# Kernel tuning notes

Hardware: AMD Instinct MI355X
Metric: run time of the kernel (lower is better)

The kernel has to match this reference:

```python
import jax, jax.numpy as jnp
import numpy as np

B, L, D = 2, 2048, 768
HEADS, KEY, HEAD = 12, 64, 64


def _glorot(key, shape):
    fan_in, fan_out = shape[0], shape[1]
    lim = jnp.sqrt(6.0 / (fan_in + fan_out))
    return jax.random.uniform(key, shape, jnp.float32, -lim, lim)


def setup_inputs() -> dict:
    key = jax.random.key(0)
    ks = jax.random.split(key, 8)
    return {
        "q": jax.random.normal(ks[0], (B, L, D), jnp.float32),
        "k": jax.random.normal(ks[1], (B, L, D), jnp.float32),
        "v": jax.random.normal(ks[2], (B, L, D), jnp.float32),
        "att_mask": jnp.ones((B, L), jnp.float32),
        "Wq": _glorot(ks[3], (D, HEADS * KEY)),
        "bq": jnp.zeros((HEADS * KEY,), jnp.float32),
        "Wk": _glorot(ks[4], (D, HEADS * KEY)),
        "bk": jnp.zeros((HEADS * KEY,), jnp.float32),
        "Wv": _glorot(ks[5], (D, HEADS * HEAD)),
        "bv": jnp.zeros((HEADS * HEAD,), jnp.float32),
        "Wo": _glorot(ks[6], (HEADS * HEAD, HEADS * HEAD)),
        "bo": jnp.zeros((HEADS * HEAD,), jnp.float32),
    }


def reference(q, k, v, att_mask, Wq, bq, Wk, bk, Wv, bv, Wo, bo):
    b, lq, _ = q.shape
    lk = k.shape[1]
    # att_mask [B,Lk] -> [B,Lq,Lk] via ones outer product (as in the TF code)
    mask2d = jnp.ones((b, lq, 1), jnp.float32) * att_mask[:, None, :]
    qh = (q @ Wq + bq).reshape(b, lq, HEADS, KEY)
    kh = (k @ Wk + bk).reshape(b, lk, HEADS, KEY)
    vh = (v @ Wv + bv).reshape(b, lk, HEADS, HEAD)
    # scores [B,H,Lq,Lk]
    a = jnp.einsum('binh,bjnh->bnij', qh, kh) / (KEY ** 0.5)
    a = a + (1.0 - mask2d[:, None, :, :]) * -99999.0
    a = jax.nn.softmax(a, axis=-1)
    o = jnp.einsum('bnij,bjnh->binh', a, vh).reshape(b, lq, HEADS * HEAD)
    return o @ Wo + bo
```

## Files before the change

kernel.cpp:

```cpp
#include <hip/hip_runtime.h>
#include <math.h>

#define BB 2
#define LL 2048
#define DD 768
#define NH 12
#define HD 64
#define EL (4096*768)
#define WEL (768*768)

typedef __attribute__((ext_vector_type(8))) short short8;
typedef __attribute__((ext_vector_type(4))) float f32x4;
typedef __attribute__((ext_vector_type(16))) float f32x16;
typedef __attribute__((ext_vector_type(4))) unsigned int u32x4;
typedef unsigned short ushortT;

union U8 { unsigned short u[8]; short8 v; };
union UB { u32x4 u; short8 v; };

#define MFMA(a,b,c)   __builtin_amdgcn_mfma_f32_16x16x32_bf16((a),(b),(c),0,0,0)
#define MFMA32(a,b,c) __builtin_amdgcn_mfma_f32_32x32x16_bf16((a),(b),(c),0,0,0)

__device__ inline unsigned short f2bf(float x) {
    unsigned int u = __float_as_uint(x);
    unsigned int r = (u + 0x7fffu + ((u >> 16) & 1u)) >> 16;
    return (unsigned short)r;
}
__device__ inline float bf2f(unsigned short s) {
    return __uint_as_float(((unsigned int)s) << 16);
}
__device__ inline void split2(float x, unsigned short& h, unsigned short& l) {
    h = f2bf(x);
    l = f2bf(x - bf2f(h));
}
__device__ inline int swz(int row) { return (((row & 7) ^ ((row >> 3) & 7)) << 4); }

__device__ inline void gl2lds16(const void* g, void* l) {
    __builtin_amdgcn_global_load_lds((__attribute__((address_space(1))) const void*)g,
                                     (__attribute__((address_space(3))) void*)l, 16, 0, 0);
}

struct SplitArgs { const float* src[3]; ushortT* dh[3]; ushortT* dl[3]; };
__global__ __launch_bounds__(256) void split_plain(SplitArgs a)
{
    const int z = blockIdx.y;
    const size_t i = ((size_t)blockIdx.x * 256 + threadIdx.x) * 8;
    const float* s = a.src[z];
    float4 v0 = *reinterpret_cast<const float4*>(s + i);
    float4 v1 = *reinterpret_cast<const float4*>(s + i + 4);
    float f[8] = {v0.x, v0.y, v0.z, v0.w, v1.x, v1.y, v1.z, v1.w};
    U8 h, l;
    #pragma unroll
    for (int j = 0; j < 8; ++j) split2(f[j], h.u[j], l.u[j]);
    *reinterpret_cast<short8*>(a.dh[z] + i) = h.v;
    *reinterpret_cast<short8*>(a.dl[z] + i) = l.v;
}

struct WArgs { const float* src[4]; ushortT* dh[4]; ushortT* dl[4]; float scale[4]; };
__global__ __launch_bounds__(256) void split_wt(WArgs a)
{
    const int n  = blockIdx.x * 256 + threadIdx.x;
    const int k0 = blockIdx.y * 8;
    const int z  = blockIdx.z;
    const float* W = a.src[z];
    const float sc = a.scale[z];
    U8 h, l;
    #pragma unroll
    for (int j = 0; j < 8; ++j) {
        float x = W[(size_t)(k0 + j) * DD + n] * sc;
        split2(x, h.u[j], l.u[j]);
    }
    *reinterpret_cast<short8*>(a.dh[z] + (size_t)n * DD + k0) = h.v;
    *reinterpret_cast<short8*>(a.dl[z] + (size_t)n * DD + k0) = l.v;
}

template<int MODE>
__global__ __launch_bounds__(256) void gemm_mfma(const ushortT* __restrict__ Ah, size_t apb,
                                                 const ushortT* __restrict__ Bth, size_t bpb,
                                                 const float* __restrict__ bias, float bscale,
                                                 float* __restrict__ outF,
                                                 ushortT* __restrict__ outH,
                                                 ushortT* __restrict__ outL)
{
    __shared__ ushortT As[64 * 64];
    __shared__ ushortT Bs[64 * 64];

    const int tid  = threadIdx.x;
    const int lane = tid & 63;
    const int w    = tid >> 6;
    const int g    = lane >> 4, c = lane & 15;
    const int n0   = blockIdx.x * 64;
    const int m0   = blockIdx.y * 64;

    const int srow0 = w * 16 + (lane >> 3);
    const int csrc  = (lane & 7) ^ (lane >> 3);
    const size_t plA = (csrc >= 4) ? apb : 0;
    const size_t plB = (csrc >= 4) ? bpb : 0;
    const size_t abase = (size_t)(m0 + srow0) * (DD * 2) + plA + (size_t)(csrc & 3) * 16;
    const size_t bbase = (size_t)(n0 + srow0) * (DD * 2) + plB + (size_t)(csrc & 3) * 16;

    f32x4 acc[4] = {{0,0,0,0},{0,0,0,0},{0,0,0,0},{0,0,0,0}};

    const int arow = w * 16 + c;
    const int ahc  = g ^ (arow & 7);
    const int aoff_h = arow * 64 + ahc * 8;
    const int aoff_l = arow * 64 + (ahc ^ 4) * 8;

    for (int kt = 0; kt < DD / 32; ++kt) {
        const size_t ko = (size_t)kt * 64;
        const char* asrc = (const char*)Ah  + abase + ko;
        const char* bsrc = (const char*)Bth + bbase + ko;
        gl2lds16(asrc,                &As[w * 1024]);
        gl2lds16(asrc + 8 * (DD * 2), &As[w * 1024 + 512]);
        gl2lds16(bsrc,                &Bs[w * 1024]);
        gl2lds16(bsrc + 8 * (DD * 2), &Bs[w * 1024 + 512]);
        __syncthreads();

        const short8 a_h = *reinterpret_cast<const short8*>(&As[aoff_h]);
        const short8 a_l = *reinterpret_cast<const short8*>(&As[aoff_l]);
        #pragma unroll
        for (int nf = 0; nf < 4; ++nf) {
            const int brow = nf * 16 + c;
            const int bhc  = g ^ (brow & 7);
            const short8 b_h = *reinterpret_cast<const short8*>(&Bs[brow * 64 + bhc * 8]);
            const short8 b_l = *reinterpret_cast<const short8*>(&Bs[brow * 64 + (bhc ^ 4) * 8]);
            acc[nf] = MFMA(a_h, b_h, acc[nf]);
            acc[nf] = MFMA(a_l, b_h, acc[nf]);
            acc[nf] = MFMA(a_h, b_l, acc[nf]);
        }
        __syncthreads();
    }

    #pragma unroll
    for (int nf = 0; nf < 4; ++nf) {
        const int n = n0 + nf * 16 + c;
        const float bz = bias[n] * bscale;
        #pragma unroll
        for (int r = 0; r < 4; ++r) {
            const int m = m0 + w * 16 + 4 * g + r;
            const float vv = acc[nf][r] + bz;
            if (MODE == 0) {
                outF[(size_t)m * DD + n] = vv;
            } else {
                unsigned short hh, ll;
                split2(vv, hh, ll);
                outH[(size_t)m * DD + n] = hh;
                outL[(size_t)m * DD + n] = ll;
            }
        }
    }
}

__global__ __launch_bounds__(128) void attn_mfma(const ushortT* __restrict__ Qh_g,
                                                 const ushortT* __restrict__ Ql_g,
                                                 const ushortT* __restrict__ Kh_g,
                                                 const ushortT* __restrict__ Kl_g,
                                                 const ushortT* __restrict__ Vh_g,
                                                 const ushortT* __restrict__ Vl_g,
                                                 const float* __restrict__ mask,
                                                 ushortT* __restrict__ Oh_g,
                                                 ushortT* __restrict__ Ol_g)
{
    __shared__ ushortT Kh[32 * 64];
    __shared__ ushortT Kl[32 * 64];
    __shared__ ushortT Vt[64 * 64];
    __shared__ float mterm[32];

    const int tid  = threadIdx.x;
    const int lane = tid & 63;
    const int w    = tid >> 6;
    const int qc   = lane & 31;
    const int h5   = lane >> 5;
    const int bh   = blockIdx.y;
    const int b    = bh / NH;
    const int h    = bh % NH;
    const int r0   = blockIdx.x * 64;
    const int qrow = r0 + w * 32 + qc;

    short8 qbh[4], qbl[4];
    {
        const size_t qoff = (size_t)(b * LL + qrow) * DD + h * 64;
        #pragma unroll
        for (int ks = 0; ks < 4; ++ks) {
            const int d0 = 8 * h5 + 16 * ks;
            qbh[ks] = *reinterpret_cast<const short8*>(Qh_g + qoff + d0);
            qbl[ks] = *reinterpret_cast<const short8*>(Ql_g + qoff + d0);
        }
    }

    f32x16 Oa[2];
    #pragma unroll
    for (int m = 0; m < 2; ++m)
        #pragma unroll
        for (int r = 0; r < 16; ++r) Oa[m][r] = 0.f;
    float mrun = -1e30f, lrun = 0.f;

    const int skey = tid >> 2;
    const int sd0v = (tid & 3) * 16;
    ushortT* kdst = w ? Kl : Kh;
    const ushortT* ksrcp = w ? Kl_g : Kh_g;
    const int krow_l = lane >> 3;
    const int kcsrc  = (lane & 7) ^ krow_l;

    for (int kt = 0; kt < LL / 32; ++kt) {
        __syncthreads();
        {
            const size_t kbase = (size_t)(b * LL + kt * 32 + krow_l) * DD + h * 64 + kcsrc * 8;
            #pragma unroll
            for (int t = 0; t < 4; ++t)
                gl2lds16(ksrcp + kbase + (size_t)(8 * t) * DD, kdst + t * 512);
        }
        {
            const size_t vo = (size_t)(b * LL + kt * 32 + skey) * DD + h * 64 + sd0v;
            U8 a0, a1, b0, b1;
            a0.v = *reinterpret_cast<const short8*>(Vh_g + vo);
            a1.v = *reinterpret_cast<const short8*>(Vh_g + vo + 8);
            b0.v = *reinterpret_cast<const short8*>(Vl_g + vo);
            b1.v = *reinterpret_cast<const short8*>(Vl_g + vo + 8);
            #pragma unroll
            for (int j = 0; j < 8; ++j) {
                int d = sd0v + j; int s = swz(d);
                Vt[d * 64 + (((2 * skey) ^ s) >> 1)]      = a0.u[j];
                Vt[d * 64 + (((64 + 2 * skey) ^ s) >> 1)] = b0.u[j];
                d = sd0v + 8 + j; s = swz(d);
                Vt[d * 64 + (((2 * skey) ^ s) >> 1)]      = a1.u[j];
                Vt[d * 64 + (((64 + 2 * skey) ^ s) >> 1)] = b1.u[j];
            }
        }
        if (tid < 32)
            mterm[tid] = (1.0f - mask[(size_t)b * LL + kt * 32 + tid]) * -99999.0f;
        __syncthreads();

        f32x16 sa;
        #pragma unroll
        for (int r = 0; r < 16; ++r) sa[r] = 0.f;
        #pragma unroll
        for (int ks = 0; ks < 4; ++ks) {
            const int ch = (h5 + 2 * ks) ^ (qc & 7);
            const short8 kfh = *reinterpret_cast<const short8*>(&Kh[qc * 64 + ch * 8]);
            const short8 kfl = *reinterpret_cast<const short8*>(&Kl[qc * 64 + ch * 8]);
            sa = MFMA32(kfh, qbh[ks], sa);
            sa = MFMA32(kfl, qbh[ks], sa);
            sa = MFMA32(kfh, qbl[ks], sa);
        }

        float sm[16];
        #pragma unroll
        for (int r = 0; r < 16; ++r)
            sm[r] = sa[r] + mterm[(r & 3) + 8 * (r >> 2) + 4 * h5];
        float tm = sm[0];
        #pragma unroll
        for (int r = 1; r < 16; ++r) tm = fmaxf(tm, sm[r]);
        tm = fmaxf(tm, __shfl_xor(tm, 32));
        const float mn = fmaxf(mrun, tm);
        const float scale = __expf(mrun - mn);
        float p[16];
        float rs = 0.f;
        #pragma unroll
        for (int r = 0; r < 16; ++r) { p[r] = __expf(sm[r] - mn); rs += p[r]; }
        rs += __shfl_xor(rs, 32);
        lrun = lrun * scale + rs;
        mrun = mn;
        #pragma unroll
        for (int m = 0; m < 2; ++m)
            #pragma unroll
            for (int r = 0; r < 16; ++r) Oa[m][r] *= scale;

        unsigned int pkh[8], pkl[8], xph[8], xpl[8];
        #pragma unroll
        for (int s2 = 0; s2 < 8; ++s2) {
            unsigned short h0, l0, h1, l1;
            split2(p[2 * s2],     h0, l0);
            split2(p[2 * s2 + 1], h1, l1);
            pkh[s2] = (unsigned int)h0 | ((unsigned int)h1 << 16);
            pkl[s2] = (unsigned int)l0 | ((unsigned int)l1 << 16);
            xph[s2] = __shfl_xor(pkh[s2], 32);
            xpl[s2] = __shfl_xor(pkl[s2], 32);
        }
        UB pbh[2], pbl[2];
        if (h5 == 0) {
            pbh[0].u = (u32x4){pkh[0], pkh[1], xph[0], xph[1]};
            pbl[0].u = (u32x4){pkl[0], pkl[1], xpl[0], xpl[1]};
            pbh[1].u = (u32x4){pkh[4], pkh[5], xph[4], xph[5]};
            pbl[1].u = (u32x4){pkl[4], pkl[5], xpl[4], xpl[5]};
        } else {
            pbh[0].u = (u32x4){xph[2], xph[3], pkh[2], pkh[3]};
            pbl[0].u = (u32x4){xpl[2], xpl[3], pkl[2], pkl[3]};
            pbh[1].u = (u32x4){xph[6], xph[7], pkh[6], pkh[7]};
            pbl[1].u = (u32x4){xpl[6], xpl[7], pkl[6], pkl[7]};
        }

        #pragma unroll
        for (int m = 0; m < 2; ++m) {
            const int d  = qc + 32 * m;
            const int sv = swz(d);
            #pragma unroll
            for (int ks2 = 0; ks2 < 2; ++ks2) {
                const int bc = 16 * h5 + 32 * ks2;
                const short8 vfh = *reinterpret_cast<const short8*>(&Vt[d * 64 + ((bc ^ sv) >> 1)]);
                const short8 vfl = *reinterpret_cast<const short8*>(&Vt[d * 64 + (((64 + bc) ^ sv) >> 1)]);
                Oa[m] = MFMA32(vfh, pbh[ks2].v, Oa[m]);
                Oa[m] = MFMA32(vfl, pbh[ks2].v, Oa[m]);
                Oa[m] = MFMA32(vfh, pbl[ks2].v, Oa[m]);
            }
        }
    }

    const float inv = 1.0f / lrun;
    const size_t obase = (size_t)(b * LL + qrow) * DD + h * 64;
    #pragma unroll
    for (int m = 0; m < 2; ++m)
        #pragma unroll
        for (int r = 0; r < 16; ++r) {
            const int d = (r & 3) + 8 * (r >> 2) + 4 * h5 + 32 * m;
            unsigned short hh, ll;
            split2(Oa[m][r] * inv, hh, ll);
            Oh_g[obase + d] = hh;
            Ol_g[obase + d] = ll;
        }
}

extern "C" void kernel_launch(void* const* d_in, const int* in_sizes, int n_in,
                              void* d_out, int out_size, void* d_ws, size_t ws_size,
                              hipStream_t stream)
{
    const float* q    = (const float*)d_in[0];
    const float* k    = (const float*)d_in[1];
    const float* v    = (const float*)d_in[2];
    const float* amask= (const float*)d_in[3];
    const float* Wq   = (const float*)d_in[4];
    const float* bq   = (const float*)d_in[5];
    const float* Wk   = (const float*)d_in[6];
    const float* bk   = (const float*)d_in[7];
    const float* Wv   = (const float*)d_in[8];
    const float* bv   = (const float*)d_in[9];
    const float* Wo   = (const float*)d_in[10];
    const float* bo   = (const float*)d_in[11];
    float* out = (float*)d_out;

    ushortT* W0 = (ushortT*)d_ws;
    ushortT* qh = W0;                 ushortT* ql = W0 + (size_t)EL;
    ushortT* kh = W0 + 2*(size_t)EL;  ushortT* kl = W0 + 3*(size_t)EL;
    ushortT* vh = W0 + 4*(size_t)EL;  ushortT* vl = W0 + 5*(size_t)EL;
    ushortT* wb = W0 + 6*(size_t)EL;
    ushortT* wqh = wb;                 ushortT* wql = wb + (size_t)WEL;
    ushortT* wkh = wb + 2*(size_t)WEL; ushortT* wkl = wb + 3*(size_t)WEL;
    ushortT* wvh = wb + 4*(size_t)WEL; ushortT* wvl = wb + 5*(size_t)WEL;
    ushortT* woh = wb + 6*(size_t)WEL; ushortT* wol = wb + 7*(size_t)WEL;
    ushortT* pb = wb + 8*(size_t)WEL;
    ushortT* Qph = pb;                 ushortT* Qpl = pb + (size_t)EL;
    ushortT* Kph = pb + 2*(size_t)EL;  ushortT* Kpl = pb + 3*(size_t)EL;
    ushortT* Vph = pb + 4*(size_t)EL;  ushortT* Vpl = pb + 5*(size_t)EL;
    ushortT* Oh = W0;                  ushortT* Ol = W0 + (size_t)EL;

    const size_t APB = (size_t)EL * 2;
    const size_t WPB = (size_t)WEL * 2;

    SplitArgs sa;
    sa.src[0] = q; sa.src[1] = k; sa.src[2] = v;
    sa.dh[0] = qh; sa.dh[1] = kh; sa.dh[2] = vh;
    sa.dl[0] = ql; sa.dl[1] = kl; sa.dl[2] = vl;
    split_plain<<<dim3(EL / 2048, 3), 256, 0, stream>>>(sa);

    WArgs wa;
    wa.src[0] = Wq; wa.src[1] = Wk; wa.src[2] = Wv; wa.src[3] = Wo;
    wa.dh[0] = wqh; wa.dh[1] = wkh; wa.dh[2] = wvh; wa.dh[3] = woh;
    wa.dl[0] = wql; wa.dl[1] = wkl; wa.dl[2] = wvl; wa.dl[3] = wol;
    wa.scale[0] = 0.125f; wa.scale[1] = 1.f; wa.scale[2] = 1.f; wa.scale[3] = 1.f;
    split_wt<<<dim3(3, 96, 4), 256, 0, stream>>>(wa);

    dim3 ggrid(DD / 64, 4096 / 64);
    gemm_mfma<1><<<ggrid, 256, 0, stream>>>(qh, APB, wqh, WPB, bq, 0.125f, nullptr, Qph, Qpl);
    gemm_mfma<1><<<ggrid, 256, 0, stream>>>(kh, APB, wkh, WPB, bk, 1.0f,   nullptr, Kph, Kpl);
    gemm_mfma<1><<<ggrid, 256, 0, stream>>>(vh, APB, wvh, WPB, bv, 1.0f,   nullptr, Vph, Vpl);

    dim3 agrid(LL / 64, BB * NH);
    attn_mfma<<<agrid, 128, 0, stream>>>(Qph, Qpl, Kph, Kpl, Vph, Vpl, amask, Oh, Ol);

    gemm_mfma<0><<<ggrid, 256, 0, stream>>>(Oh, APB, woh, WPB, bo, 1.0f, out, nullptr, nullptr);
}
```

Baseline: 388.0 us.

## Double-buffer K/V tiles in attention, batch QKV GEMMs, XCD-aware block mapping

Attention now double-buffers K and V in shared memory. It prefetches the next tile's K through direct-to-LDS loads and V into registers while computing the current tile, and it drops one barrier per iteration. The mask term for the whole row is computed once up front into a 2048-entry LDS array, and the QK accumulation is split into two independent chains. The three Q/K/V projection GEMMs are merged into one launch, and attention blocks are remapped so the blocks of a given head share an XCD. This adds LDS usage (about 40KB per block), which may reduce occupancy.

```diff
diff --git a/kernel.cpp b/kernel.cpp
--- a/kernel.cpp
+++ b/kernel.cpp
@@ -6,6 +6,7 @@
 #define DD 768
 #define NH 12
 #define HD 64
+#define NT (LL/32)
 #define EL (4096*768)
 #define WEL (768*768)
 
@@ -74,13 +75,15 @@
     *reinterpret_cast<short8*>(a.dl[z] + (size_t)n * DD + k0) = l.v;
 }
 
-template<int MODE>
-__global__ __launch_bounds__(256) void gemm_mfma(const ushortT* __restrict__ Ah, size_t apb,
-                                                 const ushortT* __restrict__ Bth, size_t bpb,
-                                                 const float* __restrict__ bias, float bscale,
-                                                 float* __restrict__ outF,
-                                                 ushortT* __restrict__ outH,
-                                                 ushortT* __restrict__ outL)
+struct QkvArgs {
+    const ushortT* A[3];
+    const ushortT* Bt[3];
+    const float* bias[3];
+    float bscale[3];
+    ushortT* oH[3];
+    ushortT* oL[3];
+};
+__global__ __launch_bounds__(256) void qkv_gemm(QkvArgs qa, size_t apb, size_t bpb)
 {
     __shared__ ushortT As[64 * 64];
     __shared__ ushortT Bs[64 * 64];
@@ -89,8 +92,13 @@
     const int lane = tid & 63;
     const int w    = tid >> 6;
     const int g    = lane >> 4, c = lane & 15;
-    const int n0   = blockIdx.x * 64;
+    const int nb   = blockIdx.x;
+    const int z    = nb / 12;
+    const int n0   = (nb % 12) * 64;
     const int m0   = blockIdx.y * 64;
+
+    const ushortT* Ah  = qa.A[z];
+    const ushortT* Bth = qa.Bt[z];
 
     const int srow0 = w * 16 + (lane >> 3);
     const int csrc  = (lane & 7) ^ (lane >> 3);
@@ -131,22 +139,86 @@
         __syncthreads();
     }
 
+    ushortT* oH = qa.oH[z];
+    ushortT* oL = qa.oL[z];
+    const float bsc = qa.bscale[z];
     #pragma unroll
     for (int nf = 0; nf < 4; ++nf) {
         const int n = n0 + nf * 16 + c;
-        const float bz = bias[n] * bscale;
+        const float bz = qa.bias[z][n] * bsc;
         #pragma unroll
         for (int r = 0; r < 4; ++r) {
             const int m = m0 + w * 16 + 4 * g + r;
-            const float vv = acc[nf][r] + bz;
-            if (MODE == 0) {
-                outF[(size_t)m * DD + n] = vv;
-            } else {
-                unsigned short hh, ll;
-                split2(vv, hh, ll);
-                outH[(size_t)m * DD + n] = hh;
-                outL[(size_t)m * DD + n] = ll;
-            }
+            unsigned short hh, ll;
+            split2(acc[nf][r] + bz, hh, ll);
+            oH[(size_t)m * DD + n] = hh;
+            oL[(size_t)m * DD + n] = ll;
+        }
+    }
+}
+
+__global__ __launch_bounds__(256) void gemm_out(const ushortT* __restrict__ Ah, size_t apb,
+                                                const ushortT* __restrict__ Bth, size_t bpb,
+                                                const float* __restrict__ bias,
+                                                float* __restrict__ outF)
+{
+    __shared__ ushortT As[64 * 64];
+    __shared__ ushortT Bs[64 * 64];
+
+    const int tid  = threadIdx.x;
+    const int lane = tid & 63;
+    const int w    = tid >> 6;
+    const int g    = lane >> 4, c = lane & 15;
+    const int n0   = blockIdx.x * 64;
+    const int m0   = blockIdx.y * 64;
+
+    const int srow0 = w * 16 + (lane >> 3);
+    const int csrc  = (lane & 7) ^ (lane >> 3);
+    const size_t plA = (csrc >= 4) ? apb : 0;
+    const size_t plB = (csrc >= 4) ? bpb : 0;
+    const size_t abase = (size_t)(m0 + srow0) * (DD * 2) + plA + (size_t)(csrc & 3) * 16;
+    const size_t bbase = (size_t)(n0 + srow0) * (DD * 2) + plB + (size_t)(csrc & 3) * 16;
+
+    f32x4 acc[4] = {{0,0,0,0},{0,0,0,0},{0,0,0,0},{0,0,0,0}};
+
+    const int arow = w * 16 + c;
+    const int ahc  = g ^ (arow & 7);
+    const int aoff_h = arow * 64 + ahc * 8;
+    const int aoff_l = arow * 64 + (ahc ^ 4) * 8;
+
+    for (int kt = 0; kt < DD / 32; ++kt) {
+        const size_t ko = (size_t)kt * 64;
+        const char* asrc = (const char*)Ah  + abase + ko;
+        const char* bsrc = (const char*)Bth + bbase + ko;
+        gl2lds16(asrc,                &As[w * 1024]);
+        gl2lds16(asrc + 8 * (DD * 2), &As[w * 1024 + 512]);
+        gl2lds16(bsrc,                &Bs[w * 1024]);
+        gl2lds16(bsrc + 8 * (DD * 2), &Bs[w * 1024 + 512]);
+        __syncthreads();
+
+        const short8 a_h = *reinterpret_cast<const short8*>(&As[aoff_h]);
+        const short8 a_l = *reinterpret_cast<const short8*>(&As[aoff_l]);
+        #pragma unroll
+        for (int nf = 0; nf < 4; ++nf) {
+            const int brow = nf * 16 + c;
+            const int bhc  = g ^ (brow & 7);
+            const short8 b_h = *reinterpret_cast<const short8*>(&Bs[brow * 64 + bhc * 8]);
+            const short8 b_l = *reinterpret_cast<const short8*>(&Bs[brow * 64 + (bhc ^ 4) * 8]);
+            acc[nf] = MFMA(a_h, b_h, acc[nf]);
+            acc[nf] = MFMA(a_l, b_h, acc[nf]);
+            acc[nf] = MFMA(a_h, b_l, acc[nf]);
+        }
+        __syncthreads();
+    }
+
+    #pragma unroll
+    for (int nf = 0; nf < 4; ++nf) {
+        const int n = n0 + nf * 16 + c;
+        const float bz = bias[n];
+        #pragma unroll
+        for (int r = 0; r < 4; ++r) {
+            const int m = m0 + w * 16 + 4 * g + r;
+            outF[(size_t)m * DD + n] = acc[nf][r] + bz;
         }
     }
 }
@@ -161,21 +233,34 @@
                                                  ushortT* __restrict__ Oh_g,
                                                  ushortT* __restrict__ Ol_g)
 {
-    __shared__ ushortT Kh[32 * 64];
-    __shared__ ushortT Kl[32 * 64];
-    __shared__ ushortT Vt[64 * 64];
-    __shared__ float mterm[32];
+    __shared__ ushortT KhS[2][32 * 64];
+    __shared__ ushortT KlS[2][32 * 64];
+    __shared__ ushortT VtS[2][64 * 64];
+    __shared__ float mterm[LL];
 
     const int tid  = threadIdx.x;
     const int lane = tid & 63;
     const int w    = tid >> 6;
     const int qc   = lane & 31;
     const int h5   = lane >> 5;
-    const int bh   = blockIdx.y;
+
+    const int wg   = blockIdx.x;
+    const int xcd  = wg & 7;
+    const int slot = wg >> 3;
+    const int bh   = xcd * 3 + (slot >> 5);
+    const int qblk = slot & 31;
     const int b    = bh / NH;
     const int h    = bh % NH;
-    const int r0   = blockIdx.x * 64;
-    const int qrow = r0 + w * 32 + qc;
+    const int qrow = qblk * 64 + w * 32 + qc;
+
+    {
+        const float* mrow = mask + (size_t)b * LL;
+        #pragma unroll
+        for (int t = 0; t < 16; ++t) {
+            const int i = tid + 128 * t;
+            mterm[i] = (1.0f - mrow[i]) * -99999.0f;
+        }
+    }
 
     short8 qbh[4], qbl[4];
     {
@@ -195,59 +280,85 @@
         for (int r = 0; r < 16; ++r) Oa[m][r] = 0.f;
     float mrun = -1e30f, lrun = 0.f;
 
-    const int skey = tid >> 2;
-    const int sd0v = (tid & 3) * 16;
-    ushortT* kdst = w ? Kl : Kh;
-    const ushortT* ksrcp = w ? Kl_g : Kh_g;
+    const int skey   = tid >> 2;
+    const int sd0v   = (tid & 3) * 16;
     const int krow_l = lane >> 3;
     const int kcsrc  = (lane & 7) ^ krow_l;
-
-    for (int kt = 0; kt < LL / 32; ++kt) {
+    const ushortT* ksrcp = w ? Kl_g : Kh_g;
+    const size_t kbase0 = (size_t)(b * LL + krow_l) * DD + h * 64 + kcsrc * 8;
+    const size_t vbase0 = (size_t)(b * LL + skey) * DD + h * 64 + sd0v;
+
+    U8 vr0, vr1, vr2, vr3;
+
+    auto KSTAGE = [&](int bufi, int kt) {
+        ushortT* kd = w ? KlS[bufi] : KhS[bufi];
+        const ushortT* ks_ = ksrcp + kbase0 + (size_t)(kt * 32) * DD;
+        #pragma unroll
+        for (int t = 0; t < 4; ++t)
+            gl2lds16(ks_ + (size_t)(8 * t) * DD, kd + t * 512);
+    };
+    auto VLOAD = [&](int kt) {
+        const ushortT* vh_ = Vh_g + vbase0 + (size_t)(kt * 32) * DD;
+        const ushortT* vl_ = Vl_g + vbase0 + (size_t)(kt * 32) * DD;
+        vr0.v = *reinterpret_cast<const short8*>(vh_);
+        vr1.v = *reinterpret_cast<const short8*>(vh_ + 8);
+        vr2.v = *reinterpret_cast<const short8*>(vl_);
+        vr3.v = *reinterpret_cast<const short8*>(vl_ + 8);
+    };
+    auto VWRITE = [&](int bufi) {
+        ushortT* vt = VtS[bufi];
+        #pragma unroll
+        for (int j = 0; j < 8; ++j) {
+            int d = sd0v + j; int s = swz(d);
+            vt[d * 64 + (((2 * skey) ^ s) >> 1)]      = vr0.u[j];
+            vt[d * 64 + (((64 + 2 * skey) ^ s) >> 1)] = vr2.u[j];
+            d = sd0v + 8 + j; s = swz(d);
+            vt[d * 64 + (((2 * skey) ^ s) >> 1)]      = vr1.u[j];
+            vt[d * 64 + (((64 + 2 * skey) ^ s) >> 1)] = vr3.u[j];
+        }
+    };
+
+    VLOAD(0);
+    KSTAGE(0, 0);
+    VWRITE(0);
+
+    for (int kt = 0; kt < NT; ++kt) {
+        const int cur = kt & 1;
         __syncthreads();
-        {
-            const size_t kbase = (size_t)(b * LL + kt * 32 + krow_l) * DD + h * 64 + kcsrc * 8;
-            #pragma unroll
-            for (int t = 0; t < 4; ++t)
-                gl2lds16(ksrcp + kbase + (size_t)(8 * t) * DD, kdst + t * 512);
-        }
-        {
-            const size_t vo = (size_t)(b * LL + kt * 32 + skey) * DD + h * 64 + sd0v;
-            U8 a0, a1, b0, b1;
-            a0.v = *reinterpret_cast<const short8*>(Vh_g + vo);
-            a1.v = *reinterpret_cast<const short8*>(Vh_g + vo + 8);
-            b0.v = *reinterpret_cast<const short8*>(Vl_g + vo);
-            b1.v = *reinterpret_cast<const short8*>(Vl_g + vo + 8);
-            #pragma unroll
-            for (int j = 0; j < 8; ++j) {
-                int d = sd0v + j; int s = swz(d);
-                Vt[d * 64 + (((2 * skey) ^ s) >> 1)]      = a0.u[j];
-                Vt[d * 64 + (((64 + 2 * skey) ^ s) >> 1)] = b0.u[j];
-                d = sd0v + 8 + j; s = swz(d);
-                Vt[d * 64 + (((2 * skey) ^ s) >> 1)]      = a1.u[j];
-                Vt[d * 64 + (((64 + 2 * skey) ^ s) >> 1)] = b1.u[j];
-            }
-        }
-        if (tid < 32)
-            mterm[tid] = (1.0f - mask[(size_t)b * LL + kt * 32 + tid]) * -99999.0f;
-        __syncthreads();
-
-        f32x16 sa;
-        #pragma unroll
-        for (int r = 0; r < 16; ++r) sa[r] = 0.f;
-        #pragma unroll
-        for (int ks = 0; ks < 4; ++ks) {
+        const bool pf = (kt + 1 < NT);
+        if (pf) {
+            KSTAGE(cur ^ 1, kt + 1);
+            VLOAD(kt + 1);
+        }
+
+        const ushortT* KhC = KhS[cur];
+        const ushortT* KlC = KlS[cur];
+        f32x16 sa0, sa1;
+        #pragma unroll
+        for (int r = 0; r < 16; ++r) { sa0[r] = 0.f; sa1[r] = 0.f; }
+        #pragma unroll
+        for (int ks = 0; ks < 2; ++ks) {
             const int ch = (h5 + 2 * ks) ^ (qc & 7);
-            const short8 kfh = *reinterpret_cast<const short8*>(&Kh[qc * 64 + ch * 8]);
-            const short8 kfl = *reinterpret_cast<const short8*>(&Kl[qc * 64 + ch * 8]);
-            sa = MFMA32(kfh, qbh[ks], sa);
-            sa = MFMA32(kfl, qbh[ks], sa);
-            sa = MFMA32(kfh, qbl[ks], sa);
+            const short8 kfh = *reinterpret_cast<const short8*>(&KhC[qc * 64 + ch * 8]);
+            const short8 kfl = *reinterpret_cast<const short8*>(&KlC[qc * 64 + ch * 8]);
+            sa0 = MFMA32(kfh, qbh[ks], sa0);
+            sa0 = MFMA32(kfl, qbh[ks], sa0);
+            sa0 = MFMA32(kfh, qbl[ks], sa0);
+        }
+        #pragma unroll
+        for (int ks = 2; ks < 4; ++ks) {
+            const int ch = (h5 + 2 * ks) ^ (qc & 7);
+            const short8 kfh = *reinterpret_cast<const short8*>(&KhC[qc * 64 + ch * 8]);
+            const short8 kfl = *reinterpret_cast<const short8*>(&KlC[qc * 64 + ch * 8]);
+            sa1 = MFMA32(kfh, qbh[ks], sa1);
+            sa1 = MFMA32(kfl, qbh[ks], sa1);
+            sa1 = MFMA32(kfh, qbl[ks], sa1);
         }
 
         float sm[16];
         #pragma unroll
         for (int r = 0; r < 16; ++r)
-            sm[r] = sa[r] + mterm[(r & 3) + 8 * (r >> 2) + 4 * h5];
+            sm[r] = sa0[r] + sa1[r] + mterm[kt * 32 + (r & 3) + 8 * (r >> 2) + 4 * h5];
         float tm = sm[0];
         #pragma unroll
         for (int r = 1; r < 16; ++r) tm = fmaxf(tm, sm[r]);
@@ -290,6 +401,7 @@
             pbl[1].u = (u32x4){xpl[6], xpl[7], pkl[6], pkl[7]};
         }
 
+        const ushortT* VtC = VtS[cur];
         #pragma unroll
         for (int m = 0; m < 2; ++m) {
             const int d  = qc + 32 * m;
@@ -297,13 +409,15 @@
             #pragma unroll
             for (int ks2 = 0; ks2 < 2; ++ks2) {
                 const int bc = 16 * h5 + 32 * ks2;
-                const short8 vfh = *reinterpret_cast<const short8*>(&Vt[d * 64 + ((bc ^ sv) >> 1)]);
-                const short8 vfl = *reinterpret_cast<const short8*>(&Vt[d * 64 + (((64 + bc) ^ sv) >> 1)]);
+                const short8 vfh = *reinterpret_cast<const short8*>(&VtC[d * 64 + ((bc ^ sv) >> 1)]);
+                const short8 vfl = *reinterpret_cast<const short8*>(&VtC[d * 64 + (((64 + bc) ^ sv) >> 1)]);
                 Oa[m] = MFMA32(vfh, pbh[ks2].v, Oa[m]);
                 Oa[m] = MFMA32(vfl, pbh[ks2].v, Oa[m]);
                 Oa[m] = MFMA32(vfh, pbl[ks2].v, Oa[m]);
             }
         }
+
+        if (pf) VWRITE(cur ^ 1);
     }
 
     const float inv = 1.0f / lrun;
@@ -369,13 +483,16 @@
     wa.scale[0] = 0.125f; wa.scale[1] = 1.f; wa.scale[2] = 1.f; wa.scale[3] = 1.f;
     split_wt<<<dim3(3, 96, 4), 256, 0, stream>>>(wa);
 
-    dim3 ggrid(DD / 64, 4096 / 64);
-    gemm_mfma<1><<<ggrid, 256, 0, stream>>>(qh, APB, wqh, WPB, bq, 0.125f, nullptr, Qph, Qpl);
-    gemm_mfma<1><<<ggrid, 256, 0, stream>>>(kh, APB, wkh, WPB, bk, 1.0f,   nullptr, Kph, Kpl);
-    gemm_mfma<1><<<ggrid, 256, 0, stream>>>(vh, APB, wvh, WPB, bv, 1.0f,   nullptr, Vph, Vpl);
-
-    dim3 agrid(LL / 64, BB * NH);
-    attn_mfma<<<agrid, 128, 0, stream>>>(Qph, Qpl, Kph, Kpl, Vph, Vpl, amask, Oh, Ol);
-
-    gemm_mfma<0><<<ggrid, 256, 0, stream>>>(Oh, APB, woh, WPB, bo, 1.0f, out, nullptr, nullptr);
-}
+    QkvArgs qa;
+    qa.A[0] = qh;  qa.A[1] = kh;  qa.A[2] = vh;
+    qa.Bt[0] = wqh; qa.Bt[1] = wkh; qa.Bt[2] = wvh;
+    qa.bias[0] = bq; qa.bias[1] = bk; qa.bias[2] = bv;
+    qa.bscale[0] = 0.125f; qa.bscale[1] = 1.f; qa.bscale[2] = 1.f;
+    qa.oH[0] = Qph; qa.oH[1] = Kph; qa.oH[2] = Vph;
+    qa.oL[0] = Qpl; qa.oL[1] = Kpl; qa.oL[2] = Vpl;
+    qkv_gemm<<<dim3(36, 64), 256, 0, stream>>>(qa, APB, WPB);
+
+    attn_mfma<<<dim3(768), 128, 0, stream>>>(Qph, Qpl, Kph, Kpl, Vph, Vpl, amask, Oh, Ol);
+
+    gemm_out<<<dim3(DD / 64, 4096 / 64), 256, 0, stream>>>(Oh, APB, woh, WPB, bo, out);
+}
```

Result: no change. 384.8 us (-0.8%).
